# Kernel tuning notes

Measured on AMD Instinct MI355X. Metric: run time of the kernel, lower is better.

## Reference

```python
import jax, jax.numpy as jnp
import numpy as np

D_HEAD = 64  # per-head dim 'd' from init_kwargs


def layer_norm(x, g, b, eps=1e-5):
    m = x.mean(-1, keepdims=True)
    v = x.var(-1, keepdims=True)  # biased var, matches torch LayerNorm
    return (x - m) / jnp.sqrt(v + eps) * g + b


def setup_inputs() -> dict:
    key = jax.random.key(0)
    ks = jax.random.split(key, 16)
    F = 512
    B, T, N = 2, 8, 1024
    s = 1.0 / np.sqrt(F)
    u = lambda k, shape: jax.random.uniform(k, shape, jnp.float32, -s, s)
    return {
        "x": jax.random.normal(ks[0], (B, T, N, F), jnp.float32),
        "Wq": u(ks[1], (F, F)), "bq": u(ks[2], (F,)),
        "Wk": u(ks[3], (F, F)), "bk": u(ks[4], (F,)),
        "Wv": u(ks[5], (F, F)), "bv": u(ks[6], (F,)),
        "ln_g": jnp.ones((F,), jnp.float32), "ln_b": jnp.zeros((F,), jnp.float32),
        "W1": u(ks[7], (F, F)), "b1": u(ks[8], (F,)),
        "W2": u(ks[9], (F, F)), "b2": u(ks[10], (F,)),
        "lnff_g": jnp.ones((F,), jnp.float32), "lnff_b": jnp.zeros((F,), jnp.float32),
    }


def reference(x, Wq, bq, Wk, bk, Wv, bv, ln_g, ln_b, W1, b1, W2, b2, lnff_g, lnff_b):
    B, T, N, F = x.shape
    h = F // D_HEAD
    # q/k/v projections
    q = x @ Wq + bq
    k = x @ Wk + bk
    v = x @ Wv + bv
    # split last dim into heads (split+cat(dim=0) in torch == head axis here)
    qh = q.reshape(B, T, N, h, D_HEAD)
    kh = k.reshape(B, T, N, h, D_HEAD)
    vh = v.reshape(B, T, N, h, D_HEAD)
    # attention over node axis N per (batch, time, head)
    A = jnp.einsum('btqhd,btkhd->bthqk', qh, kh) / jnp.sqrt(jnp.asarray(D_HEAD, x.dtype))
    A = jax.nn.softmax(A, axis=-1)
    o = jnp.einsum('bthqk,btkhd->btqhd', A, vh).reshape(B, T, N, F)
    # residual + LN
    val = layer_norm(o + x, ln_g, ln_b)
    # FFN + final LN
    ff = jax.nn.relu(val @ W1 + b1) @ W2 + b2
    return layer_norm(ff, lnff_g, lnff_b)
```

## Files before the change

### kernel.cpp

```cpp
#include <hip/hip_runtime.h>
#include <hip/hip_bf16.h>

using bf16 = __hip_bfloat16;
typedef unsigned int u32x4 __attribute__((ext_vector_type(4)));
typedef float f32x4 __attribute__((ext_vector_type(4)));
typedef __bf16 bf16x8 __attribute__((ext_vector_type(8)));

#define DEVI __device__ __forceinline__

DEVI f32x4 mfma16(u32x4 a, u32x4 b, f32x4 c) {
    return __builtin_amdgcn_mfma_f32_16x16x32_bf16(
        __builtin_bit_cast(bf16x8, a), __builtin_bit_cast(bf16x8, b), c, 0, 0, 0);
}

DEVI void gload16(const bf16* g, bf16* l) {
    __builtin_amdgcn_global_load_lds(
        (const __attribute__((address_space(1))) unsigned int*)g,
        (__attribute__((address_space(3))) unsigned int*)l,
        16, 0, 0);
}

struct bf8 { bf16 h[8]; };

DEVI u32x4 pack8(f32x4 lo, f32x4 hi) {
    bf8 t;
#pragma unroll
    for (int i = 0; i < 4; i++) {
        t.h[i] = __float2bfloat16(lo[i]);
        t.h[4 + i] = __float2bfloat16(hi[i]);
    }
    return __builtin_bit_cast(u32x4, t);
}

DEVI unsigned long long pk4(float a, float b, float c, float d) {
    union { unsigned long long u; bf16 h[4]; } t;
    t.h[0] = __float2bfloat16(a); t.h[1] = __float2bfloat16(b);
    t.h[2] = __float2bfloat16(c); t.h[3] = __float2bfloat16(d);
    return t.u;
}

DEVI unsigned trunc2(float a, float b) {
    return __builtin_amdgcn_perm(__builtin_bit_cast(unsigned, b),
                                 __builtin_bit_cast(unsigned, a), 0x07060302);
}

__global__ __launch_bounds__(256) void prep(
    const float* __restrict__ Wq, const float* __restrict__ Wk,
    const float* __restrict__ Wv, const float* __restrict__ W1,
    const float* __restrict__ W2, const float* __restrict__ x,
    bf16* __restrict__ WT, bf16* __restrict__ xb)
{
    int b = blockIdx.x;
    if (b < 5120) {
        int w = b >> 10;
        const float* src = (w == 0) ? Wq : (w == 1) ? Wk : (w == 2) ? Wv : (w == 3) ? W1 : W2;
        int idx = (b & 1023) * 256 + threadIdx.x;
        int n = idx >> 9, kk = idx & 511;
        WT[(size_t)w * 262144 + idx] = __float2bfloat16(src[kk * 512 + n]);
    } else {
        size_t i = ((size_t)(b - 5120) * 256 + threadIdx.x) * 8;
        f32x4 lo = *(const f32x4*)&x[i];
        f32x4 hi = *(const f32x4*)&x[i + 4];
        *(u32x4*)&xb[i] = pack8(lo, hi);
    }
}

#define GEMM_BODY(EPILOGUE)                                                          \
    __shared__ __align__(16) bf16 As[128 * 64];                                      \
    __shared__ __align__(16) bf16 Bs[128 * 64];                                      \
    const int tid = threadIdx.x;                                                     \
    const int lane = tid & 63, wave = tid >> 6;                                      \
    const int wm = (wave >> 1) * 64, wn = (wave & 1) * 64;                           \
    const int lm = lane & 15, lq = lane >> 4;                                        \
    const int cxor = (lm & 7) * 8;                                                   \
    const int srow = wave * 32 + (lane >> 3);                                        \
    const int scol = ((lane & 7) ^ (lane >> 3)) * 8;                                 \
    const bf16* Ag = A + (size_t)(bm + srow) * 512 + scol;                           \
    const bf16* Bg = Bt + (size_t)(bn + srow) * 512 + scol;                          \
    bf16* Al = &As[wave * 32 * 64];                                                  \
    bf16* Bl = &Bs[wave * 32 * 64];                                                  \
    f32x4 acc[4][4];                                                                 \
    _Pragma("unroll") for (int i = 0; i < 4; i++)                                    \
        _Pragma("unroll") for (int j = 0; j < 4; j++)                                \
            acc[i][j] = (f32x4){0.f, 0.f, 0.f, 0.f};                                 \
    for (int k0 = 0; k0 < 512; k0 += 64) {                                           \
        __syncthreads();                   \
        _Pragma("unroll") for (int p = 0; p < 4; p++) {                              \
            gload16(Ag + (size_t)p * 8 * 512 + k0, Al + p * 512);                    \
            gload16(Bg + (size_t)p * 8 * 512 + k0, Bl + p * 512);                    \
        }                                                                            \
        __syncthreads();                   \
        _Pragma("unroll") for (int h = 0; h < 2; h++) {                              \
            u32x4 af[4], bfr[4];                                                     \
            _Pragma("unroll") for (int i = 0; i < 4; i++)                            \
                af[i] = *(const u32x4*)&As[(wm + i * 16 + lm) * 64 + ((h * 32 + lq * 8) ^ cxor)]; \
            _Pragma("unroll") for (int j = 0; j < 4; j++)                            \
                bfr[j] = *(const u32x4*)&Bs[(wn + j * 16 + lm) * 64 + ((h * 32 + lq * 8) ^ cxor)]; \
            EPILOGUE##_MMA                                                           \
        }                                                                            \
    }

#define SWAPPED_MMA                                                                  \
    _Pragma("unroll") for (int i = 0; i < 4; i++)                                    \
        _Pragma("unroll") for (int j = 0; j < 4; j++)                                \
            acc[i][j] = mfma16(bfr[j], af[i], acc[i][j]);

#define GEMM_BODY_N64(EPILOGUE)                                                      \
    __shared__ __align__(16) bf16 As[128 * 64];                                      \
    __shared__ __align__(16) bf16 Bs[64 * 64];                                       \
    const int tid = threadIdx.x;                                                     \
    const int lane = tid & 63, wave = tid >> 6;                                      \
    const int wm = wave * 32;                                                        \
    const int lm = lane & 15, lq = lane >> 4;                                        \
    const int cxor = (lm & 7) * 8;                                                   \
    const int sr8 = lane >> 3;                                                       \
    const int scol = ((lane & 7) ^ sr8) * 8;                                         \
    const bf16* Ag = A + (size_t)(bm + wave * 32 + sr8) * 512 + scol;                \
    const bf16* Bg = Bt + (size_t)(bn + wave * 16 + sr8) * 512 + scol;               \
    bf16* Al = &As[wave * 32 * 64];                                                  \
    bf16* Bl = &Bs[wave * 16 * 64];                                                  \
    f32x4 acc[2][4];                                                                 \
    _Pragma("unroll") for (int i = 0; i < 2; i++)                                    \
        _Pragma("unroll") for (int j = 0; j < 4; j++)                                \
            acc[i][j] = (f32x4){0.f, 0.f, 0.f, 0.f};                                 \
    for (int k0 = 0; k0 < 512; k0 += 64) {                                           \
        __syncthreads();                                                             \
        _Pragma("unroll") for (int p = 0; p < 4; p++)                                \
            gload16(Ag + (size_t)p * 8 * 512 + k0, Al + p * 512);                    \
        _Pragma("unroll") for (int p = 0; p < 2; p++)                                \
            gload16(Bg + (size_t)p * 8 * 512 + k0, Bl + p * 512);                    \
        __syncthreads();                                                             \
        _Pragma("unroll") for (int h = 0; h < 2; h++) {                              \
            u32x4 af[2], bfr[4];                                                     \
            _Pragma("unroll") for (int i = 0; i < 2; i++)                            \
                af[i] = *(const u32x4*)&As[(wm + i * 16 + lm) * 64 + ((h * 32 + lq * 8) ^ cxor)]; \
            _Pragma("unroll") for (int j = 0; j < 4; j++)                            \
                bfr[j] = *(const u32x4*)&Bs[(j * 16 + lm) * 64 + ((h * 32 + lq * 8) ^ cxor)]; \
            EPILOGUE##_MMA_N64                                                       \
        }                                                                            \
    }

#define SWAPPED_MMA_N64                                                              \
    _Pragma("unroll") for (int i = 0; i < 2; i++)                                    \
        _Pragma("unroll") for (int j = 0; j < 4; j++)                                \
            acc[i][j] = mfma16(bfr[j], af[i], acc[i][j]);
#define NORMAL_MMA_N64                                                               \
    _Pragma("unroll") for (int i = 0; i < 2; i++)                                    \
        _Pragma("unroll") for (int j = 0; j < 4; j++)                                \
            acc[i][j] = mfma16(af[i], bfr[j], acc[i][j]);

__global__ __launch_bounds__(256) void gemm_qk(
    const bf16* __restrict__ A, const bf16* __restrict__ WT,
    const float* __restrict__ bqp, const float* __restrict__ bkp,
    bf16* __restrict__ qb, bf16* __restrict__ kb)
{
    const int wsel = blockIdx.y >> 2;
    const int bm = blockIdx.x * 128, bn = (blockIdx.y & 3) * 128;
    const bf16* Bt = WT + (size_t)wsel * 262144;
    const float* bias = (wsel == 0) ? bqp : bkp;
    const float scale = (wsel == 0) ? 0.18033688f : 1.0f;
    bf16* dst = (wsel == 0) ? qb : kb;

    GEMM_BODY(SWAPPED)
#pragma unroll
    for (int i = 0; i < 4; i++) {
#pragma unroll
        for (int j = 0; j < 4; j++) {
            int row = bm + wm + i * 16 + lm;
            int colb = bn + wn + j * 16 + lq * 4;
            f32x4 b4 = *(const f32x4*)&bias[colb];
            *(unsigned long long*)&dst[(size_t)row * 512 + colb] =
                pk4((acc[i][j][0] + b4[0]) * scale, (acc[i][j][1] + b4[1]) * scale,
                    (acc[i][j][2] + b4[2]) * scale, (acc[i][j][3] + b4[3]) * scale);
        }
    }
}

__global__ __launch_bounds__(256) void gemm_v(
    const bf16* __restrict__ A, const bf16* __restrict__ WT,
    const float* __restrict__ bvp, bf16* __restrict__ vT)
{
    const int bm = blockIdx.x * 128, bn = blockIdx.y * 64;
    const bf16* Bt = WT + (size_t)2 * 262144;
    const float* bias = bvp;

    GEMM_BODY_N64(NORMAL)
#pragma unroll
    for (int i = 0; i < 2; i++) {
#pragma unroll
        for (int j = 0; j < 4; j++) {
            int col = bn + j * 16 + lm;
            float bv = bias[col];
            int rowb = bm + wm + i * 16 + lq * 4;
            int btq = rowb >> 10, node = rowb & 1023;
            int u = node & 31;
            int nodeP = (node & ~31) | (((u >> 2) & 3) << 3) | (((u >> 4) & 1) << 2);
            *(unsigned long long*)&vT[((size_t)((btq * 8 + (col >> 6)) * 64 + (col & 63))) * 1024 + nodeP] =
                pk4(acc[i][j][0] + bv, acc[i][j][1] + bv,
                    acc[i][j][2] + bv, acc[i][j][3] + bv);
        }
    }
}

template <bool RELU>
__global__ __launch_bounds__(256) void gemm_bt(
    const bf16* __restrict__ A, const bf16* __restrict__ Bt,
    const float* __restrict__ bias, bf16* __restrict__ C)
{
    const int bm = blockIdx.x * 128, bn = blockIdx.y * 64;
    GEMM_BODY_N64(SWAPPED)
#pragma unroll
    for (int i = 0; i < 2; i++) {
#pragma unroll
        for (int j = 0; j < 4; j++) {
            int row = bm + wm + i * 16 + lm;
            int colb = bn + j * 16 + lq * 4;
            f32x4 b4 = *(const f32x4*)&bias[colb];
            float c0 = acc[i][j][0] + b4[0], c1 = acc[i][j][1] + b4[1];
            float c2 = acc[i][j][2] + b4[2], c3 = acc[i][j][3] + b4[3];
            if (RELU) {
                c0 = fmaxf(c0, 0.f); c1 = fmaxf(c1, 0.f);
                c2 = fmaxf(c2, 0.f); c3 = fmaxf(c3, 0.f);
            }
            *(unsigned long long*)&C[(size_t)row * 512 + colb] = pk4(c0, c1, c2, c3);
        }
    }
}

__global__ __launch_bounds__(256, 4) void attn_kernel(
    const bf16* __restrict__ q, const bf16* __restrict__ k,
    const bf16* __restrict__ vT, float* __restrict__ o)
{
    constexpr int KP = 72;
    constexpr int VP = 72;
    __shared__ __align__(16) bf16 Ks[2][64 * KP];
    __shared__ __align__(16) bf16 Vs[2][64 * VP];

    const int tid = threadIdx.x, lane = tid & 63, wave = tid >> 6;
    const int group = blockIdx.x;
    const int bt = group >> 3, hh = group & 7;
    const int lm = lane & 15, lq = lane >> 4;
    const int qrow0 = bt * 1024 + blockIdx.y * 128 + wave * 32;

    u32x4 qf[2][2];
#pragma unroll
    for (int tm = 0; tm < 2; tm++)
#pragma unroll
        for (int kk2 = 0; kk2 < 2; kk2++)
            qf[tm][kk2] = *(const u32x4*)&q[(size_t)(qrow0 + tm * 16 + lm) * 512 + hh * 64 + kk2 * 32 + lq * 8];

    const bf16* kbase = k + (size_t)(bt * 1024) * 512 + hh * 64;
    const bf16* vbase = vT + (size_t)group * 64 * 1024;

    const int r0 = tid >> 3, e0 = (tid & 7) * 8;
    const int r1 = (256 + tid) >> 3;

    const unsigned ow = (lm == 0) ? 0x3F803F80u : 0u;
    const u32x4 onesA = (u32x4){ow, ow, ow, ow};

    f32x4 accO[4][2];
#pragma unroll
    for (int md = 0; md < 4; md++)
#pragma unroll
        for (int tm = 0; tm < 2; tm++) accO[md][tm] = (f32x4){0.f, 0.f, 0.f, 0.f};
    f32x4 accL[2] = {(f32x4){0.f, 0.f, 0.f, 0.f}, (f32x4){0.f, 0.f, 0.f, 0.f}};

    u32x4 kreg0 = *(const u32x4*)&kbase[(size_t)r0 * 512 + e0];
    u32x4 kreg1 = *(const u32x4*)&kbase[(size_t)r1 * 512 + e0];
    u32x4 vreg0 = *(const u32x4*)&vbase[(size_t)r0 * 1024 + e0];
    u32x4 vreg1 = *(const u32x4*)&vbase[(size_t)r1 * 1024 + e0];

    for (int kt = 0; kt < 16; kt++) {
        bf16* Kb = Ks[kt & 1];
        bf16* Vb = Vs[kt & 1];
        *(u32x4*)&Kb[r0 * KP + e0] = kreg0;
        *(u32x4*)&Kb[r1 * KP + e0] = kreg1;
        *(u32x4*)&Vb[r0 * VP + e0] = vreg0;
        *(u32x4*)&Vb[r1 * VP + e0] = vreg1;
        __syncthreads();
        if (kt < 15) {
            const bf16* kn = kbase + (size_t)((kt + 1) * 64) * 512;
            const bf16* vn = vbase + (kt + 1) * 64;
            kreg0 = *(const u32x4*)&kn[(size_t)r0 * 512 + e0];
            kreg1 = *(const u32x4*)&kn[(size_t)r1 * 512 + e0];
            vreg0 = *(const u32x4*)&vn[(size_t)r0 * 1024 + e0];
            vreg1 = *(const u32x4*)&vn[(size_t)r1 * 1024 + e0];
        }

#pragma unroll
        for (int kc = 0; kc < 2; kc++) {
            const int t0 = kc * 2;
            u32x4 kf00 = *(const u32x4*)&Kb[(t0 * 16 + lm) * KP + lq * 8];
            u32x4 kf01 = *(const u32x4*)&Kb[(t0 * 16 + lm) * KP + 32 + lq * 8];
            u32x4 kf10 = *(const u32x4*)&Kb[((t0 + 1) * 16 + lm) * KP + lq * 8];
            u32x4 kf11 = *(const u32x4*)&Kb[((t0 + 1) * 16 + lm) * KP + 32 + lq * 8];
            u32x4 pw[2];
#pragma unroll
            for (int tm = 0; tm < 2; tm++) {
                f32x4 s0 = (f32x4){0.f, 0.f, 0.f, 0.f};
                s0 = mfma16(kf00, qf[tm][0], s0);
                s0 = mfma16(kf01, qf[tm][1], s0);
                f32x4 s1 = (f32x4){0.f, 0.f, 0.f, 0.f};
                s1 = mfma16(kf10, qf[tm][0], s1);
                s1 = mfma16(kf11, qf[tm][1], s1);
                float p0 = __builtin_amdgcn_exp2f(s0[0]);
                float p1 = __builtin_amdgcn_exp2f(s0[1]);
                float p2 = __builtin_amdgcn_exp2f(s0[2]);
                float p3 = __builtin_amdgcn_exp2f(s0[3]);
                float p4 = __builtin_amdgcn_exp2f(s1[0]);
                float p5 = __builtin_amdgcn_exp2f(s1[1]);
                float p6 = __builtin_amdgcn_exp2f(s1[2]);
                float p7 = __builtin_amdgcn_exp2f(s1[3]);
                pw[tm] = (u32x4){trunc2(p0, p1), trunc2(p2, p3),
                                 trunc2(p4, p5), trunc2(p6, p7)};
            }
            accL[0] = mfma16(onesA, pw[0], accL[0]);
            accL[1] = mfma16(onesA, pw[1], accL[1]);
            __builtin_amdgcn_s_setprio(1);
#pragma unroll
            for (int md = 0; md < 4; md++) {
                u32x4 vf = *(const u32x4*)&Vb[(md * 16 + lm) * VP + kc * 32 + lq * 8];
                accO[md][0] = mfma16(vf, pw[0], accO[md][0]);
                accO[md][1] = mfma16(vf, pw[1], accO[md][1]);
            }
            __builtin_amdgcn_s_setprio(0);
        }
    }

#pragma unroll
    for (int tm = 0; tm < 2; tm++) {
        float l = accL[tm][0];
        l += __shfl_xor(l, 16);
        l += __shfl_xor(l, 32);
        float linv = 1.0f / l;
#pragma unroll
        for (int md = 0; md < 4; md++) {
            f32x4 r;
#pragma unroll
            for (int i = 0; i < 4; i++) r[i] = accO[md][tm][i] * linv;
            *(f32x4*)&o[(size_t)(qrow0 + tm * 16 + lm) * 512 + hh * 64 + md * 16 + lq * 4] = r;
        }
    }
}

template <bool AF32, bool RES, bool OF32>
__global__ __launch_bounds__(256) void ln_kernel(
    const void* __restrict__ a, const float* __restrict__ res,
    const float* __restrict__ g, const float* __restrict__ bb, void* __restrict__ out)
{
    int row = blockIdx.x * 4 + (threadIdx.x >> 6);
    int lane = threadIdx.x & 63;
    size_t base = (size_t)row * 512 + lane * 8;
    int cbase = lane * 8;

    float x8[8];
    if (AF32) {
        const float* af = (const float*)a;
        f32x4 lo = *(const f32x4*)&af[base];
        f32x4 hi = *(const f32x4*)&af[base + 4];
#pragma unroll
        for (int i = 0; i < 4; i++) { x8[i] = lo[i]; x8[4 + i] = hi[i]; }
    } else {
        bf8 av = __builtin_bit_cast(bf8, *(const u32x4*)&((const bf16*)a)[base]);
#pragma unroll
        for (int i = 0; i < 8; i++) x8[i] = __bfloat162float(av.h[i]);
    }
    if (RES) {
        f32x4 lo = *(const f32x4*)&res[base];
        f32x4 hi = *(const f32x4*)&res[base + 4];
#pragma unroll
        for (int i = 0; i < 4; i++) { x8[i] += lo[i]; x8[4 + i] += hi[i]; }
    }

    float s = 0.f, s2 = 0.f;
#pragma unroll
    for (int i = 0; i < 8; i++) { s += x8[i]; s2 += x8[i] * x8[i]; }
#pragma unroll
    for (int off = 1; off < 64; off <<= 1) {
        s += __shfl_xor(s, off);
        s2 += __shfl_xor(s2, off);
    }
    float mean = s * (1.f / 512.f);
    float var = s2 * (1.f / 512.f) - mean * mean;
    float rstd = rsqrtf(var + 1e-5f);

    f32x4 g0 = *(const f32x4*)&g[cbase], g1 = *(const f32x4*)&g[cbase + 4];
    f32x4 b0 = *(const f32x4*)&bb[cbase], b1v = *(const f32x4*)&bb[cbase + 4];
    float y[8];
#pragma unroll
    for (int i = 0; i < 4; i++) {
        y[i] = (x8[i] - mean) * rstd * g0[i] + b0[i];
        y[4 + i] = (x8[4 + i] - mean) * rstd * g1[i] + b1v[i];
    }
    if (OF32) {
        float* op = (float*)out;
        *(f32x4*)&op[base] = (f32x4){y[0], y[1], y[2], y[3]};
        *(f32x4*)&op[base + 4] = (f32x4){y[4], y[5], y[6], y[7]};
    } else {
        bf8 ov;
#pragma unroll
        for (int i = 0; i < 8; i++) ov.h[i] = __float2bfloat16(y[i]);
        *(u32x4*)&((bf16*)out)[base] = __builtin_bit_cast(u32x4, ov);
    }
}

extern "C" void kernel_launch(void* const* d_in, const int* in_sizes, int n_in,
                              void* d_out, int out_size, void* d_ws, size_t ws_size,
                              hipStream_t stream)
{
    const float* x    = (const float*)d_in[0];
    const float* Wq   = (const float*)d_in[1];
    const float* bq   = (const float*)d_in[2];
    const float* Wk   = (const float*)d_in[3];
    const float* bk   = (const float*)d_in[4];
    const float* Wv   = (const float*)d_in[5];
    const float* bv   = (const float*)d_in[6];
    const float* ln_g = (const float*)d_in[7];
    const float* ln_b = (const float*)d_in[8];
    const float* W1   = (const float*)d_in[9];
    const float* b1   = (const float*)d_in[10];
    const float* W2   = (const float*)d_in[11];
    const float* b2   = (const float*)d_in[12];
    const float* lnffg = (const float*)d_in[13];
    const float* lnffb = (const float*)d_in[14];
    float* out = (float*)d_out;

    bf16* ws = (bf16*)d_ws;
    bf16* WT = ws;
    bf16* qb = ws + 5 * 262144;
    bf16* kb = qb + 8388608;
    bf16* vT = kb + 8388608;
    bf16* vl = qb;
    bf16* f1 = kb;
    bf16* f2 = vT;
    bf16* xb = (bf16*)d_out;

    prep<<<9216, 256, 0, stream>>>(Wq, Wk, Wv, W1, W2, x, WT, xb);

    gemm_qk<<<dim3(128, 8), 256, 0, stream>>>(xb, WT, bq, bk, qb, kb);
    gemm_v <<<dim3(128, 8), 256, 0, stream>>>(xb, WT, bv, vT);

    attn_kernel<<<dim3(128, 8), 256, 0, stream>>>(qb, kb, vT, out);

    ln_kernel<true, true, false><<<4096, 256, 0, stream>>>(out, x, ln_g, ln_b, vl);

    dim3 gg(128, 8);
    gemm_bt<true> <<<gg, 256, 0, stream>>>(vl, WT + 3 * 262144, b1, f1);
    gemm_bt<false><<<gg, 256, 0, stream>>>(f1, WT + 4 * 262144, b2, f2);

    ln_kernel<false, false, true><<<4096, 256, 0, stream>>>(f2, nullptr, lnffg, lnffb, out);
}
```

Before: 241.7 us.

## Fuse attention with residual-add LayerNorm, one block handling all heads per row tile

The attention kernel is restructured so that each 512-thread block owns 32 query rows across all 8 heads, with one wave per head. K and V tiles are loaded straight into LDS with global_load_lds, using 32-key steps and a single buffer in place of the old register-staged double buffer. Because a block now holds whole rows, the residual add and the first LayerNorm run in the epilogue through a cross-wave reduction in shared memory. This removes the fp32 attention-output round trip and the separate LN kernel. The cost is less latency hiding inside the K/V loop, two barriers per iteration, and a one-pass variance formula.

```diff
diff --git a/kernel.cpp b/kernel.cpp
--- a/kernel.cpp
+++ b/kernel.cpp
@@ -21,6 +21,7 @@
 }
 
 struct bf8 { bf16 h[8]; };
+struct f2 { float x, y; };
 
 DEVI u32x4 pack8(f32x4 lo, f32x4 hi) {
     bf8 t;
@@ -84,12 +85,12 @@
         _Pragma("unroll") for (int j = 0; j < 4; j++)                                \
             acc[i][j] = (f32x4){0.f, 0.f, 0.f, 0.f};                                 \
     for (int k0 = 0; k0 < 512; k0 += 64) {                                           \
-        __syncthreads();                   \
+        __syncthreads();                                                             \
         _Pragma("unroll") for (int p = 0; p < 4; p++) {                              \
             gload16(Ag + (size_t)p * 8 * 512 + k0, Al + p * 512);                    \
             gload16(Bg + (size_t)p * 8 * 512 + k0, Bl + p * 512);                    \
         }                                                                            \
-        __syncthreads();                   \
+        __syncthreads();                                                             \
         _Pragma("unroll") for (int h = 0; h < 2; h++) {                              \
             u32x4 af[4], bfr[4];                                                     \
             _Pragma("unroll") for (int i = 0; i < 4; i++)                            \
@@ -227,33 +228,32 @@
     }
 }
 
-__global__ __launch_bounds__(256, 4) void attn_kernel(
+__global__ __launch_bounds__(512) void attn_ln(
     const bf16* __restrict__ q, const bf16* __restrict__ k,
-    const bf16* __restrict__ vT, float* __restrict__ o)
-{
-    constexpr int KP = 72;
-    constexpr int VP = 72;
-    __shared__ __align__(16) bf16 Ks[2][64 * KP];
-    __shared__ __align__(16) bf16 Vs[2][64 * VP];
-
-    const int tid = threadIdx.x, lane = tid & 63, wave = tid >> 6;
-    const int group = blockIdx.x;
-    const int bt = group >> 3, hh = group & 7;
+    const bf16* __restrict__ vT, const float* __restrict__ x,
+    const float* __restrict__ lng, const float* __restrict__ lnb,
+    bf16* __restrict__ vl)
+{
+    __shared__ __align__(16) bf16 Ks[32 * 512];
+    __shared__ __align__(16) bf16 Vs[8 * 64 * 32];
+
+    const int tid = threadIdx.x, lane = tid & 63, w = tid >> 6;
+    const int bt = blockIdx.x;
     const int lm = lane & 15, lq = lane >> 4;
-    const int qrow0 = bt * 1024 + blockIdx.y * 128 + wave * 32;
+    const int qrow0 = bt * 1024 + blockIdx.y * 32;
+    const int swz = (lm & 7) * 8;
 
     u32x4 qf[2][2];
 #pragma unroll
     for (int tm = 0; tm < 2; tm++)
 #pragma unroll
         for (int kk2 = 0; kk2 < 2; kk2++)
-            qf[tm][kk2] = *(const u32x4*)&q[(size_t)(qrow0 + tm * 16 + lm) * 512 + hh * 64 + kk2 * 32 + lq * 8];
-
-    const bf16* kbase = k + (size_t)(bt * 1024) * 512 + hh * 64;
-    const bf16* vbase = vT + (size_t)group * 64 * 1024;
-
-    const int r0 = tid >> 3, e0 = (tid & 7) * 8;
-    const int r1 = (256 + tid) >> 3;
+            qf[tm][kk2] = *(const u32x4*)&q[(size_t)(qrow0 + tm * 16 + lm) * 512 + w * 64 + kk2 * 32 + lq * 8];
+
+    const bf16* kp = k + (size_t)(bt * 1024 + w) * 512 + ((lane ^ w) * 8);
+    const bf16* vp = vT + ((size_t)((bt * 8 + (w >> 2)) * 64 + (w & 3) * 16 + (lane >> 2))) * 1024 + (lane & 3) * 8;
+    bf16* kl = &Ks[w * 512];
+    bf16* vld = &Vs[w * 512];
 
     const unsigned ow = (lm == 0) ? 0x3F803F80u : 0u;
     const u32x4 onesA = (u32x4){ow, ow, ow, ow};
@@ -265,80 +265,104 @@
         for (int tm = 0; tm < 2; tm++) accO[md][tm] = (f32x4){0.f, 0.f, 0.f, 0.f};
     f32x4 accL[2] = {(f32x4){0.f, 0.f, 0.f, 0.f}, (f32x4){0.f, 0.f, 0.f, 0.f}};
 
-    u32x4 kreg0 = *(const u32x4*)&kbase[(size_t)r0 * 512 + e0];
-    u32x4 kreg1 = *(const u32x4*)&kbase[(size_t)r1 * 512 + e0];
-    u32x4 vreg0 = *(const u32x4*)&vbase[(size_t)r0 * 1024 + e0];
-    u32x4 vreg1 = *(const u32x4*)&vbase[(size_t)r1 * 1024 + e0];
-
-    for (int kt = 0; kt < 16; kt++) {
-        bf16* Kb = Ks[kt & 1];
-        bf16* Vb = Vs[kt & 1];
-        *(u32x4*)&Kb[r0 * KP + e0] = kreg0;
-        *(u32x4*)&Kb[r1 * KP + e0] = kreg1;
-        *(u32x4*)&Vb[r0 * VP + e0] = vreg0;
-        *(u32x4*)&Vb[r1 * VP + e0] = vreg1;
+    for (int kt = 0; kt < 32; kt++) {
         __syncthreads();
-        if (kt < 15) {
-            const bf16* kn = kbase + (size_t)((kt + 1) * 64) * 512;
-            const bf16* vn = vbase + (kt + 1) * 64;
-            kreg0 = *(const u32x4*)&kn[(size_t)r0 * 512 + e0];
-            kreg1 = *(const u32x4*)&kn[(size_t)r1 * 512 + e0];
-            vreg0 = *(const u32x4*)&vn[(size_t)r0 * 1024 + e0];
-            vreg1 = *(const u32x4*)&vn[(size_t)r1 * 1024 + e0];
-        }
-
-#pragma unroll
-        for (int kc = 0; kc < 2; kc++) {
-            const int t0 = kc * 2;
-            u32x4 kf00 = *(const u32x4*)&Kb[(t0 * 16 + lm) * KP + lq * 8];
-            u32x4 kf01 = *(const u32x4*)&Kb[(t0 * 16 + lm) * KP + 32 + lq * 8];
-            u32x4 kf10 = *(const u32x4*)&Kb[((t0 + 1) * 16 + lm) * KP + lq * 8];
-            u32x4 kf11 = *(const u32x4*)&Kb[((t0 + 1) * 16 + lm) * KP + 32 + lq * 8];
-            u32x4 pw[2];
-#pragma unroll
-            for (int tm = 0; tm < 2; tm++) {
-                f32x4 s0 = (f32x4){0.f, 0.f, 0.f, 0.f};
-                s0 = mfma16(kf00, qf[tm][0], s0);
-                s0 = mfma16(kf01, qf[tm][1], s0);
-                f32x4 s1 = (f32x4){0.f, 0.f, 0.f, 0.f};
-                s1 = mfma16(kf10, qf[tm][0], s1);
-                s1 = mfma16(kf11, qf[tm][1], s1);
-                float p0 = __builtin_amdgcn_exp2f(s0[0]);
-                float p1 = __builtin_amdgcn_exp2f(s0[1]);
-                float p2 = __builtin_amdgcn_exp2f(s0[2]);
-                float p3 = __builtin_amdgcn_exp2f(s0[3]);
-                float p4 = __builtin_amdgcn_exp2f(s1[0]);
-                float p5 = __builtin_amdgcn_exp2f(s1[1]);
-                float p6 = __builtin_amdgcn_exp2f(s1[2]);
-                float p7 = __builtin_amdgcn_exp2f(s1[3]);
-                pw[tm] = (u32x4){trunc2(p0, p1), trunc2(p2, p3),
-                                 trunc2(p4, p5), trunc2(p6, p7)};
-            }
-            accL[0] = mfma16(onesA, pw[0], accL[0]);
-            accL[1] = mfma16(onesA, pw[1], accL[1]);
-            __builtin_amdgcn_s_setprio(1);
-#pragma unroll
-            for (int md = 0; md < 4; md++) {
-                u32x4 vf = *(const u32x4*)&Vb[(md * 16 + lm) * VP + kc * 32 + lq * 8];
-                accO[md][0] = mfma16(vf, pw[0], accO[md][0]);
-                accO[md][1] = mfma16(vf, pw[1], accO[md][1]);
-            }
-            __builtin_amdgcn_s_setprio(0);
-        }
-    }
-
+#pragma unroll
+        for (int p = 0; p < 4; p++) {
+            gload16(kp + (size_t)kt * 16384 + p * 4096, kl + p * 4096);
+            gload16(vp + kt * 32 + (size_t)p * 131072, vld + p * 4096);
+        }
+        __syncthreads();
+
+        u32x4 kf00 = *(const u32x4*)&Ks[(size_t)lm * 512 + w * 64 + ((lq * 8) ^ swz)];
+        u32x4 kf01 = *(const u32x4*)&Ks[(size_t)lm * 512 + w * 64 + ((32 + lq * 8) ^ swz)];
+        u32x4 kf10 = *(const u32x4*)&Ks[(size_t)(16 + lm) * 512 + w * 64 + ((lq * 8) ^ swz)];
+        u32x4 kf11 = *(const u32x4*)&Ks[(size_t)(16 + lm) * 512 + w * 64 + ((32 + lq * 8) ^ swz)];
+        u32x4 pw[2];
+#pragma unroll
+        for (int tm = 0; tm < 2; tm++) {
+            f32x4 s0 = (f32x4){0.f, 0.f, 0.f, 0.f};
+            s0 = mfma16(kf00, qf[tm][0], s0);
+            s0 = mfma16(kf01, qf[tm][1], s0);
+            f32x4 s1 = (f32x4){0.f, 0.f, 0.f, 0.f};
+            s1 = mfma16(kf10, qf[tm][0], s1);
+            s1 = mfma16(kf11, qf[tm][1], s1);
+            float p0 = __builtin_amdgcn_exp2f(s0[0]);
+            float p1 = __builtin_amdgcn_exp2f(s0[1]);
+            float p2 = __builtin_amdgcn_exp2f(s0[2]);
+            float p3 = __builtin_amdgcn_exp2f(s0[3]);
+            float p4 = __builtin_amdgcn_exp2f(s1[0]);
+            float p5 = __builtin_amdgcn_exp2f(s1[1]);
+            float p6 = __builtin_amdgcn_exp2f(s1[2]);
+            float p7 = __builtin_amdgcn_exp2f(s1[3]);
+            pw[tm] = (u32x4){trunc2(p0, p1), trunc2(p2, p3),
+                             trunc2(p4, p5), trunc2(p6, p7)};
+        }
+        accL[0] = mfma16(onesA, pw[0], accL[0]);
+        accL[1] = mfma16(onesA, pw[1], accL[1]);
+        __builtin_amdgcn_s_setprio(1);
+#pragma unroll
+        for (int md = 0; md < 4; md++) {
+            u32x4 vf = *(const u32x4*)&Vs[w * 2048 + (md * 16 + lm) * 32 + lq * 8];
+            accO[md][0] = mfma16(vf, pw[0], accO[md][0]);
+            accO[md][1] = mfma16(vf, pw[1], accO[md][1]);
+        }
+        __builtin_amdgcn_s_setprio(0);
+    }
+
+    float sP[2], s2P[2];
 #pragma unroll
     for (int tm = 0; tm < 2; tm++) {
         float l = accL[tm][0];
         l += __shfl_xor(l, 16);
         l += __shfl_xor(l, 32);
         float linv = 1.0f / l;
+        float s = 0.f, s2 = 0.f;
 #pragma unroll
         for (int md = 0; md < 4; md++) {
-            f32x4 r;
-#pragma unroll
-            for (int i = 0; i < 4; i++) r[i] = accO[md][tm][i] * linv;
-            *(f32x4*)&o[(size_t)(qrow0 + tm * 16 + lm) * 512 + hh * 64 + md * 16 + lq * 4] = r;
+            f32x4 xv = *(const f32x4*)&x[(size_t)(qrow0 + tm * 16 + lm) * 512 + w * 64 + md * 16 + lq * 4];
+            f32x4 t;
+#pragma unroll
+            for (int i = 0; i < 4; i++) {
+                t[i] = accO[md][tm][i] * linv + xv[i];
+                s += t[i];
+                s2 += t[i] * t[i];
+            }
+            accO[md][tm] = t;
+        }
+        s += __shfl_xor(s, 16);  s += __shfl_xor(s, 32);
+        s2 += __shfl_xor(s2, 16); s2 += __shfl_xor(s2, 32);
+        sP[tm] = s; s2P[tm] = s2;
+    }
+    __syncthreads();
+    f2* sred = (f2*)Ks;
+    if (lq == 0) {
+        sred[(w * 2 + 0) * 16 + lm] = f2{sP[0], s2P[0]};
+        sred[(w * 2 + 1) * 16 + lm] = f2{sP[1], s2P[1]};
+    }
+    __syncthreads();
+#pragma unroll
+    for (int tm = 0; tm < 2; tm++) {
+        float S = 0.f, S2 = 0.f;
+#pragma unroll
+        for (int wj = 0; wj < 8; wj++) {
+            f2 v = sred[(wj * 2 + tm) * 16 + lm];
+            S += v.x; S2 += v.y;
+        }
+        float mean = S * (1.f / 512.f);
+        float var = S2 * (1.f / 512.f) - mean * mean;
+        float rstd = rsqrtf(var + 1e-5f);
+#pragma unroll
+        for (int md = 0; md < 4; md++) {
+            int colb = w * 64 + md * 16 + lq * 4;
+            f32x4 g4 = *(const f32x4*)&lng[colb];
+            f32x4 b4 = *(const f32x4*)&lnb[colb];
+            f32x4 t = accO[md][tm];
+            *(unsigned long long*)&vl[(size_t)(qrow0 + tm * 16 + lm) * 512 + colb] =
+                pk4((t[0] - mean) * rstd * g4[0] + b4[0],
+                    (t[1] - mean) * rstd * g4[1] + b4[1],
+                    (t[2] - mean) * rstd * g4[2] + b4[2],
+                    (t[3] - mean) * rstd * g4[3] + b4[3]);
         }
     }
 }
@@ -440,9 +464,7 @@
     gemm_qk<<<dim3(128, 8), 256, 0, stream>>>(xb, WT, bq, bk, qb, kb);
     gemm_v <<<dim3(128, 8), 256, 0, stream>>>(xb, WT, bv, vT);
 
-    attn_kernel<<<dim3(128, 8), 256, 0, stream>>>(qb, kb, vT, out);
-
-    ln_kernel<true, true, false><<<4096, 256, 0, stream>>>(out, x, ln_g, ln_b, vl);
+    attn_ln<<<dim3(16, 32), 512, 0, stream>>>(qb, kb, vT, x, ln_g, ln_b, vl);
 
     dim3 gg(128, 8);
     gemm_bt<true> <<<gg, 256, 0, stream>>>(vl, WT + 3 * 262144, b1, f1);
```

Measured after the change: 258.4 us. 6.9% more time.

## Halve attention query tile per block and single-buffer K/V shared memory

Applied to the files above, without the earlier changes.

The attention kernel now gives each wave 16 query rows instead of 32, so a block covers 64 queries and the grid doubles along y to 16. K/V shared tiles go from double to single buffering, with an extra barrier before each tile store. This raises block count and occupancy and lowers register and LDS use. In exchange, every K/V tile is loaded from global/L2 twice as often, and the added barrier serialises stores with the previous compute.

```diff
diff --git a/kernel.cpp b/kernel.cpp
--- a/kernel.cpp
+++ b/kernel.cpp
@@ -84,12 +84,12 @@
         _Pragma("unroll") for (int j = 0; j < 4; j++)                                \
             acc[i][j] = (f32x4){0.f, 0.f, 0.f, 0.f};                                 \
     for (int k0 = 0; k0 < 512; k0 += 64) {                                           \
-        __syncthreads();                   \
+        __syncthreads();                                                             \
         _Pragma("unroll") for (int p = 0; p < 4; p++) {                              \
             gload16(Ag + (size_t)p * 8 * 512 + k0, Al + p * 512);                    \
             gload16(Bg + (size_t)p * 8 * 512 + k0, Bl + p * 512);                    \
         }                                                                            \
-        __syncthreads();                   \
+        __syncthreads();                                                             \
         _Pragma("unroll") for (int h = 0; h < 2; h++) {                              \
             u32x4 af[4], bfr[4];                                                     \
             _Pragma("unroll") for (int i = 0; i < 4; i++)                            \
@@ -233,21 +233,19 @@
 {
     constexpr int KP = 72;
     constexpr int VP = 72;
-    __shared__ __align__(16) bf16 Ks[2][64 * KP];
-    __shared__ __align__(16) bf16 Vs[2][64 * VP];
+    __shared__ __align__(16) bf16 Ks[64 * KP];
+    __shared__ __align__(16) bf16 Vs[64 * VP];
 
     const int tid = threadIdx.x, lane = tid & 63, wave = tid >> 6;
     const int group = blockIdx.x;
     const int bt = group >> 3, hh = group & 7;
     const int lm = lane & 15, lq = lane >> 4;
-    const int qrow0 = bt * 1024 + blockIdx.y * 128 + wave * 32;
-
-    u32x4 qf[2][2];
-#pragma unroll
-    for (int tm = 0; tm < 2; tm++)
-#pragma unroll
-        for (int kk2 = 0; kk2 < 2; kk2++)
-            qf[tm][kk2] = *(const u32x4*)&q[(size_t)(qrow0 + tm * 16 + lm) * 512 + hh * 64 + kk2 * 32 + lq * 8];
+    const int qrow0 = bt * 1024 + blockIdx.y * 64 + wave * 16;
+
+    u32x4 qf[2];
+#pragma unroll
+    for (int kk2 = 0; kk2 < 2; kk2++)
+        qf[kk2] = *(const u32x4*)&q[(size_t)(qrow0 + lm) * 512 + hh * 64 + kk2 * 32 + lq * 8];
 
     const bf16* kbase = k + (size_t)(bt * 1024) * 512 + hh * 64;
     const bf16* vbase = vT + (size_t)group * 64 * 1024;
@@ -258,12 +256,10 @@
     const unsigned ow = (lm == 0) ? 0x3F803F80u : 0u;
     const u32x4 onesA = (u32x4){ow, ow, ow, ow};
 
-    f32x4 accO[4][2];
-#pragma unroll
-    for (int md = 0; md < 4; md++)
-#pragma unroll
-        for (int tm = 0; tm < 2; tm++) accO[md][tm] = (f32x4){0.f, 0.f, 0.f, 0.f};
-    f32x4 accL[2] = {(f32x4){0.f, 0.f, 0.f, 0.f}, (f32x4){0.f, 0.f, 0.f, 0.f}};
+    f32x4 accO[4];
+#pragma unroll
+    for (int md = 0; md < 4; md++) accO[md] = (f32x4){0.f, 0.f, 0.f, 0.f};
+    f32x4 accL = (f32x4){0.f, 0.f, 0.f, 0.f};
 
     u32x4 kreg0 = *(const u32x4*)&kbase[(size_t)r0 * 512 + e0];
     u32x4 kreg1 = *(const u32x4*)&kbase[(size_t)r1 * 512 + e0];
@@ -271,12 +267,11 @@
     u32x4 vreg1 = *(const u32x4*)&vbase[(size_t)r1 * 1024 + e0];
 
     for (int kt = 0; kt < 16; kt++) {
-        bf16* Kb = Ks[kt & 1];
-        bf16* Vb = Vs[kt & 1];
-        *(u32x4*)&Kb[r0 * KP + e0] = kreg0;
-        *(u32x4*)&Kb[r1 * KP + e0] = kreg1;
-        *(u32x4*)&Vb[r0 * VP + e0] = vreg0;
-        *(u32x4*)&Vb[r1 * VP + e0] = vreg1;
+        __syncthreads();
+        *(u32x4*)&Ks[r0 * KP + e0] = kreg0;
+        *(u32x4*)&Ks[r1 * KP + e0] = kreg1;
+        *(u32x4*)&Vs[r0 * VP + e0] = vreg0;
+        *(u32x4*)&Vs[r1 * VP + e0] = vreg1;
         __syncthreads();
         if (kt < 15) {
             const bf16* kn = kbase + (size_t)((kt + 1) * 64) * 512;
@@ -290,56 +285,47 @@
 #pragma unroll
         for (int kc = 0; kc < 2; kc++) {
             const int t0 = kc * 2;
-            u32x4 kf00 = *(const u32x4*)&Kb[(t0 * 16 + lm) * KP + lq * 8];
-            u32x4 kf01 = *(const u32x4*)&Kb[(t0 * 16 + lm) * KP + 32 + lq * 8];
-            u32x4 kf10 = *(const u32x4*)&Kb[((t0 + 1) * 16 + lm) * KP + lq * 8];
-            u32x4 kf11 = *(const u32x4*)&Kb[((t0 + 1) * 16 + lm) * KP + 32 + lq * 8];
-            u32x4 pw[2];
-#pragma unroll
-            for (int tm = 0; tm < 2; tm++) {
-                f32x4 s0 = (f32x4){0.f, 0.f, 0.f, 0.f};
-                s0 = mfma16(kf00, qf[tm][0], s0);
-                s0 = mfma16(kf01, qf[tm][1], s0);
-                f32x4 s1 = (f32x4){0.f, 0.f, 0.f, 0.f};
-                s1 = mfma16(kf10, qf[tm][0], s1);
-                s1 = mfma16(kf11, qf[tm][1], s1);
-                float p0 = __builtin_amdgcn_exp2f(s0[0]);
-                float p1 = __builtin_amdgcn_exp2f(s0[1]);
-                float p2 = __builtin_amdgcn_exp2f(s0[2]);
-                float p3 = __builtin_amdgcn_exp2f(s0[3]);
-                float p4 = __builtin_amdgcn_exp2f(s1[0]);
-                float p5 = __builtin_amdgcn_exp2f(s1[1]);
-                float p6 = __builtin_amdgcn_exp2f(s1[2]);
-                float p7 = __builtin_amdgcn_exp2f(s1[3]);
-                pw[tm] = (u32x4){trunc2(p0, p1), trunc2(p2, p3),
-                                 trunc2(p4, p5), trunc2(p6, p7)};
-            }
-            accL[0] = mfma16(onesA, pw[0], accL[0]);
-            accL[1] = mfma16(onesA, pw[1], accL[1]);
+            u32x4 kf00 = *(const u32x4*)&Ks[(t0 * 16 + lm) * KP + lq * 8];
+            u32x4 kf01 = *(const u32x4*)&Ks[(t0 * 16 + lm) * KP + 32 + lq * 8];
+            u32x4 kf10 = *(const u32x4*)&Ks[((t0 + 1) * 16 + lm) * KP + lq * 8];
+            u32x4 kf11 = *(const u32x4*)&Ks[((t0 + 1) * 16 + lm) * KP + 32 + lq * 8];
+            f32x4 s0 = (f32x4){0.f, 0.f, 0.f, 0.f};
+            s0 = mfma16(kf00, qf[0], s0);
+            s0 = mfma16(kf01, qf[1], s0);
+            f32x4 s1 = (f32x4){0.f, 0.f, 0.f, 0.f};
+            s1 = mfma16(kf10, qf[0], s1);
+            s1 = mfma16(kf11, qf[1], s1);
+            float p0 = __builtin_amdgcn_exp2f(s0[0]);
+            float p1 = __builtin_amdgcn_exp2f(s0[1]);
+            float p2 = __builtin_amdgcn_exp2f(s0[2]);
+            float p3 = __builtin_amdgcn_exp2f(s0[3]);
+            float p4 = __builtin_amdgcn_exp2f(s1[0]);
+            float p5 = __builtin_amdgcn_exp2f(s1[1]);
+            float p6 = __builtin_amdgcn_exp2f(s1[2]);
+            float p7 = __builtin_amdgcn_exp2f(s1[3]);
+            u32x4 pw = (u32x4){trunc2(p0, p1), trunc2(p2, p3),
+                               trunc2(p4, p5), trunc2(p6, p7)};
+            accL = mfma16(onesA, pw, accL);
             __builtin_amdgcn_s_setprio(1);
 #pragma unroll
             for (int md = 0; md < 4; md++) {
-                u32x4 vf = *(const u32x4*)&Vb[(md * 16 + lm) * VP + kc * 32 + lq * 8];
-                accO[md][0] = mfma16(vf, pw[0], accO[md][0]);
-                accO[md][1] = mfma16(vf, pw[1], accO[md][1]);
+                u32x4 vf = *(const u32x4*)&Vs[(md * 16 + lm) * VP + kc * 32 + lq * 8];
+                accO[md] = mfma16(vf, pw, accO[md]);
             }
             __builtin_amdgcn_s_setprio(0);
         }
     }
 
-#pragma unroll
-    for (int tm = 0; tm < 2; tm++) {
-        float l = accL[tm][0];
-        l += __shfl_xor(l, 16);
-        l += __shfl_xor(l, 32);
-        float linv = 1.0f / l;
-#pragma unroll
-        for (int md = 0; md < 4; md++) {
-            f32x4 r;
-#pragma unroll
-            for (int i = 0; i < 4; i++) r[i] = accO[md][tm][i] * linv;
-            *(f32x4*)&o[(size_t)(qrow0 + tm * 16 + lm) * 512 + hh * 64 + md * 16 + lq * 4] = r;
-        }
+    float l = accL[0];
+    l += __shfl_xor(l, 16);
+    l += __shfl_xor(l, 32);
+    float linv = 1.0f / l;
+#pragma unroll
+    for (int md = 0; md < 4; md++) {
+        f32x4 r;
+#pragma unroll
+        for (int i = 0; i < 4; i++) r[i] = accO[md][i] * linv;
+        *(f32x4*)&o[(size_t)(qrow0 + lm) * 512 + hh * 64 + md * 16 + lq * 4] = r;
     }
 }
 
@@ -440,7 +426,7 @@
     gemm_qk<<<dim3(128, 8), 256, 0, stream>>>(xb, WT, bq, bk, qb, kb);
     gemm_v <<<dim3(128, 8), 256, 0, stream>>>(xb, WT, bv, vT);
 
-    attn_kernel<<<dim3(128, 8), 256, 0, stream>>>(qb, kb, vT, out);
+    attn_kernel<<<dim3(128, 16), 256, 0, stream>>>(qb, kb, vT, out);
 
     ln_kernel<true, true, false><<<4096, 256, 0, stream>>>(out, x, ln_g, ln_b, vl);
 
```

After: 257.8 us. 1.07x slower.
